# Performance work log

Hardware: AMD Instinct MI355X
Metric: run time of the kernel (lower is better)

Reference implementation:

```python
import jax, jax.numpy as jnp
import numpy as np

PAST = 15        # sum(num_classes[:-1])
NC = 20          # sum(num_classes)
ALPHA = 0.99
IGNORE = 255


def setup_inputs() -> dict:
    key = jax.random.key(0)
    k1, k2, k3, k4, k5, k6 = jax.random.split(key, 6)
    B, C, H, W = 8, NC, 512, 512
    logit = jax.random.normal(k1, (B, C, H, W), dtype=jnp.float32)
    # ema_prob is used as probabilities (gathered & compared to thresholds)
    ema_prob = jax.nn.softmax(jax.random.normal(k2, (B, C, H, W), dtype=jnp.float32), axis=1)
    ema_thresh = jax.random.uniform(k3, (NC,), dtype=jnp.float32, minval=0.2, maxval=0.8)
    real_labels = jax.random.randint(k4, (B, H, W), 0, NC, dtype=jnp.int64)
    # sprinkle ignore pixels (255) like real segmentation masks
    real_labels = jnp.where(jax.random.uniform(k5, (B, H, W)) < 0.1, IGNORE, real_labels)
    moving_prob_avg = jax.random.uniform(k6, (NC,), dtype=jnp.float32)
    return {"logit": logit, "ema_prob": ema_prob, "ema_thresh": ema_thresh,
            "real_labels": real_labels, "moving_prob_avg": moving_prob_avg}


def reference(logit, ema_prob, ema_thresh, real_labels, moving_prob_avg):
    # --- pseudo-labels from current model (detached softmax) ---
    logit_prob = jax.nn.softmax(jax.lax.stop_gradient(logit), axis=1)  # [B,C,H,W]
    labels = jnp.argmax(logit_prob[:, :PAST], axis=1)                   # [B,H,W]
    labels = jnp.where(real_labels >= PAST, real_labels, labels)
    idx = jnp.where(real_labels == IGNORE, 0, labels)
    scores = jnp.take_along_axis(logit_prob, idx[:, None], axis=1)[:, 0]  # [B,H,W]

    # --- per-class mean of scores + EMA update of moving_prob_avg ---
    flat_lab = labels.reshape(-1)
    flat_sc = scores.reshape(-1)
    seg = jnp.where(flat_lab == IGNORE, NC, flat_lab)  # route ignored to extra bucket
    sums = jax.ops.segment_sum(flat_sc, seg, num_segments=NC + 1)[:NC]
    counts = jax.ops.segment_sum(jnp.ones_like(flat_sc), seg, num_segments=NC + 1)[:NC]
    means = sums / jnp.maximum(counts, 1.0)
    mpa = moving_prob_avg  # numpy buffer in torch (no grad)
    new_mpa = jnp.where(counts > 0,
                        jnp.where(mpa == -1.0, means, (1.0 - ALPHA) * means + ALPHA * mpa),
                        mpa)

    # --- EMA-teacher pseudo labels + threshold mask ---
    ema_labels = jnp.argmax(ema_prob[:, :PAST], axis=1)
    ema_labels = jnp.where(real_labels >= PAST, real_labels, ema_labels)
    eidx = jnp.where(real_labels == IGNORE, 0, ema_labels)
    ema_scores = jnp.take_along_axis(ema_prob, eidx[:, None], axis=1)[:, 0]
    valid_cls = ema_labels < NC  # 255 never matches any class in the torch loop
    thr = ema_thresh[jnp.clip(ema_labels, 0, NC - 1)]
    ema_mask = valid_cls & (ema_scores >= thr)
    dynamic_labels = jnp.where(ema_mask, ema_labels, IGNORE)  # [B,H,W]

    # --- masked cross-entropy with per-class reweighting ---
    logp = jax.nn.log_softmax(logit, axis=1)
    cidx = jnp.clip(dynamic_labels, 0, NC - 1)
    losses = -jnp.take_along_axis(logp, cidx[:, None], axis=1)[:, 0]
    valid = dynamic_labels != IGNORE
    mult = jnp.where(valid, 1.0 - new_mpa[cidx], 1.0)
    losses = losses * jax.lax.stop_gradient(mult)  # multiplier is a host scalar in torch
    vs = valid.astype(losses.dtype)
    return jnp.sum(losses * vs) / jnp.sum(vs)
```

## Files before the change

kernel.cpp:

```cpp
#include <hip/hip_runtime.h>
#include <math.h>


#define PASTC 15
#define NCC   20
#define IGN   255
#define HW2   262144
#define ALPHAF 0.99f

#define TPX   256
#define NBLK  1024
#define ITER  8

typedef const __attribute__((address_space(1))) void* gp1_t;
typedef __attribute__((address_space(3))) void*       sp3_t;

__global__ __launch_bounds__(256) void dl_main(
    const float* __restrict__ logit,
    const float* __restrict__ ema,
    const float* __restrict__ thresh,
    const int*   __restrict__ real,
    float*       __restrict__ ws)
{
    __shared__ float stage[40 * TPX];
    __shared__ float s_acc[61];

    const int tid = threadIdx.x;
    const int wv  = tid >> 6;
    const int ln  = tid & 63;
    if (tid < 61) s_acc[tid] = 0.0f;

    for (int it = 0; it < ITER; ++it) {
        const int tile = blockIdx.x * ITER + it;
        const int p0   = tile * TPX;
        const int b    = p0 >> 18;
        const int s0   = p0 & (HW2 - 1);
        const size_t cb = ((size_t)(b * NCC) << 18) + (size_t)s0;

#pragma unroll
        for (int k = 0; k < 10; ++k) {
            const int e  = wv * 10 + k;
            const int tn = (e >= NCC);
            const int ch = tn ? (e - NCC) : e;
            const float* src = (tn ? ema : logit) + cb + ((size_t)ch << 18)
                             + (size_t)ln * 4;
            __builtin_amdgcn_global_load_lds((gp1_t)src, (sp3_t)&stage[e * TPX],
                                             16, 0, 0);
        }
        const int rl = real[p0 + tid];

        __syncthreads();

        const float* le = &stage[NCC * TPX];

        float e_m15 = le[tid]; int e_arg = 0;
#pragma unroll
        for (int c = 1; c < PASTC; ++c) {
            const float v = le[c * TPX + tid];
            if (v > e_m15) { e_m15 = v; e_arg = c; }
        }
        const int   el  = (rl >= PASTC) ? rl : e_arg;
        const float esc = (rl == IGN) ? le[tid]
                        : ((rl >= PASTC) ? le[rl * TPX + tid] : e_m15);
        const float th  = thresh[el < NCC ? el : (NCC - 1)];
        const bool  valid = (el < NCC) && (esc >= th);
        const int   cidx  = valid ? el : -1;

        float m20 = stage[tid], m15 = stage[tid]; int arg15 = 0;
#pragma unroll
        for (int c = 1; c < NCC; ++c) {
            const float v = stage[c * TPX + tid];
            if (c < PASTC && v > m15) { m15 = v; arg15 = c; }
            m20 = fmaxf(m20, v);
        }
        float se = 0.0f;
#pragma unroll
        for (int c = 0; c < NCC; ++c)
            se += __expf(stage[c * TPX + tid] - m20);
        const float lse = m20 + __logf(se);

        if (rl != IGN) {
            const int   lab  = (rl >= PASTC) ? rl : arg15;
            const float sval = (rl >= PASTC) ? stage[rl * TPX + tid] : m15;
            const float prob = __expf(sval - lse);
            atomicAdd(&s_acc[lab], prob);
            atomicAdd(&s_acc[20 + lab], 1.0f);
        }
        if (cidx >= 0) {
            const float capL = stage[cidx * TPX + tid];
            atomicAdd(&s_acc[40 + cidx], lse - capL);
        }
        const unsigned long long bm = __ballot(cidx >= 0);
        if (ln == 0) atomicAdd(&s_acc[60], (float)__popcll(bm));

        __syncthreads();
    }

    if (tid < 61) atomicAdd(&ws[tid], s_acc[tid]);
}

__global__ void dl_final(const float* __restrict__ ws,
                         const float* __restrict__ mpa,
                         float*       __restrict__ out)
{
    if (threadIdx.x == 0 && blockIdx.x == 0) {
        float acc = 0.0f;
        for (int c = 0; c < NCC; ++c) {
            const float ssum = ws[c];
            const float cnt  = ws[20 + c];
            const float lsum = ws[40 + c];
            const float m    = mpa[c];
            const float mean = ssum / fmaxf(cnt, 1.0f);
            const float nm   = (cnt > 0.0f)
                                 ? ((m == -1.0f) ? mean
                                                 : (1.0f - ALPHAF) * mean + ALPHAF * m)
                                 : m;
            acc += lsum * (1.0f - nm);
        }
        out[0] = acc / ws[60];
    }
}

extern "C" void kernel_launch(void* const* d_in, const int* in_sizes, int n_in,
                              void* d_out, int out_size, void* d_ws, size_t ws_size,
                              hipStream_t stream) {
    const float* logit  = (const float*)d_in[0];
    const float* ema    = (const float*)d_in[1];
    const float* thresh = (const float*)d_in[2];
    const int*   real   = (const int*)d_in[3];
    const float* mpa    = (const float*)d_in[4];
    float* out = (float*)d_out;
    float* ws  = (float*)d_ws;

    hipMemsetAsync(ws, 0, 64 * sizeof(float), stream);

    dl_main<<<NBLK, 256, 0, stream>>>(logit, ema, thresh, real, ws);
    dl_final<<<1, 64, 0, stream>>>(ws, mpa, out);
}
```

Baseline: 367.5 us.

## Split staging into separate ema and logit buffers and software-pipeline their loads

New measurement: 376.9 us. 2.5% more time.

```diff
diff --git a/kernel.cpp b/kernel.cpp
--- a/kernel.cpp
+++ b/kernel.cpp
@@ -15,6 +15,9 @@
 typedef const __attribute__((address_space(1))) void* gp1_t;
 typedef __attribute__((address_space(3))) void*       sp3_t;
 
+#define BARSYNC() asm volatile("s_waitcnt lgkmcnt(0)\n\ts_barrier" ::: "memory")
+#define WAITV(n)  asm volatile("s_waitcnt vmcnt(" #n ")" ::: "memory")
+
 __global__ __launch_bounds__(256) void dl_main(
     const float* __restrict__ logit,
     const float* __restrict__ ema,
@@ -22,80 +25,110 @@
     const int*   __restrict__ real,
     float*       __restrict__ ws)
 {
-    __shared__ float stage[40 * TPX];
+    __shared__ float bufE[NCC * TPX];
+    __shared__ float bufL[NCC * TPX];
+    __shared__ int   realrow[TPX];
     __shared__ float s_acc[61];
+    __shared__ float s_th[NCC];
 
     const int tid = threadIdx.x;
     const int wv  = tid >> 6;
     const int ln  = tid & 63;
-    if (tid < 61) s_acc[tid] = 0.0f;
+    if (tid < 61)  s_acc[tid] = 0.0f;
+    if (tid < NCC) s_th[tid]  = thresh[tid];
 
-    for (int it = 0; it < ITER; ++it) {
-        const int tile = blockIdx.x * ITER + it;
-        const int p0   = tile * TPX;
-        const int b    = p0 >> 18;
-        const int s0   = p0 & (HW2 - 1);
+    auto issue_ema = [&](int tile) {
+        const int p0 = tile * TPX;
+        const int b  = p0 >> 18;
+        const int s0 = p0 & (HW2 - 1);
         const size_t cb = ((size_t)(b * NCC) << 18) + (size_t)s0;
+#pragma unroll
+        for (int k2 = 0; k2 < 5; ++k2) {
+            const int ch = wv * 5 + k2;
+            const float* src = ema + cb + ((size_t)ch << 18) + (size_t)ln * 4;
+            __builtin_amdgcn_global_load_lds((gp1_t)src, (sp3_t)&bufE[ch * TPX], 16, 0, 0);
+        }
+        const int* rsrc = real + p0 + wv * 64 + ln;
+        __builtin_amdgcn_global_load_lds((gp1_t)rsrc, (sp3_t)&realrow[wv * 64], 4, 0, 0);
+    };
+    auto issue_logit = [&](int tile) {
+        const int p0 = tile * TPX;
+        const int b  = p0 >> 18;
+        const int s0 = p0 & (HW2 - 1);
+        const size_t cb = ((size_t)(b * NCC) << 18) + (size_t)s0;
+#pragma unroll
+        for (int k2 = 0; k2 < 5; ++k2) {
+            const int ch = wv * 5 + k2;
+            const float* src = logit + cb + ((size_t)ch << 18) + (size_t)ln * 4;
+            __builtin_amdgcn_global_load_lds((gp1_t)src, (sp3_t)&bufL[ch * TPX], 16, 0, 0);
+        }
+    };
 
-#pragma unroll
-        for (int k = 0; k < 10; ++k) {
-            const int e  = wv * 10 + k;
-            const int tn = (e >= NCC);
-            const int ch = tn ? (e - NCC) : e;
-            const float* src = (tn ? ema : logit) + cb + ((size_t)ch << 18)
-                             + (size_t)ln * 4;
-            __builtin_amdgcn_global_load_lds((gp1_t)src, (sp3_t)&stage[e * TPX],
-                                             16, 0, 0);
-        }
-        const int rl = real[p0 + tid];
+    const int t0 = blockIdx.x * ITER;
+    issue_ema(t0);
 
-        __syncthreads();
+    int   rl = 0, cidx = -1;
 
-        const float* le = &stage[NCC * TPX];
+    for (int k = 0; k < ITER; ++k) {
+        issue_logit(t0 + k);
+        WAITV(5);
+        BARSYNC();
 
-        float e_m15 = le[tid]; int e_arg = 0;
+        rl = realrow[tid];
+        float e_m15 = bufE[tid]; int e_arg = 0;
 #pragma unroll
         for (int c = 1; c < PASTC; ++c) {
-            const float v = le[c * TPX + tid];
+            const float v = bufE[c * TPX + tid];
             if (v > e_m15) { e_m15 = v; e_arg = c; }
         }
-        const int   el  = (rl >= PASTC) ? rl : e_arg;
-        const float esc = (rl == IGN) ? le[tid]
-                        : ((rl >= PASTC) ? le[rl * TPX + tid] : e_m15);
-        const float th  = thresh[el < NCC ? el : (NCC - 1)];
-        const bool  valid = (el < NCC) && (esc >= th);
-        const int   cidx  = valid ? el : -1;
+        {
+            const int   el  = (rl >= PASTC) ? rl : e_arg;
+            const int   gch = (rl == IGN) ? 0 : ((rl >= PASTC) ? rl : 0);
+            const float gv  = bufE[gch * TPX + tid];
+            const float esc = (rl != IGN && rl < PASTC) ? e_m15 : gv;
+            const float th  = s_th[el < NCC ? el : (NCC - 1)];
+            cidx = ((el < NCC) && (esc >= th)) ? el : -1;
+        }
+        BARSYNC();
 
-        float m20 = stage[tid], m15 = stage[tid]; int arg15 = 0;
+        if (k < ITER - 1) { issue_ema(t0 + k + 1); WAITV(6); }
+        else              { WAITV(0); }
+        BARSYNC();
+
+        float m20 = bufL[tid], m15v = bufL[tid]; int arg15 = 0;
 #pragma unroll
         for (int c = 1; c < NCC; ++c) {
-            const float v = stage[c * TPX + tid];
-            if (c < PASTC && v > m15) { m15 = v; arg15 = c; }
+            const float v = bufL[c * TPX + tid];
+            if (c < PASTC && v > m15v) { m15v = v; arg15 = c; }
             m20 = fmaxf(m20, v);
         }
         float se = 0.0f;
 #pragma unroll
         for (int c = 0; c < NCC; ++c)
-            se += __expf(stage[c * TPX + tid] - m20);
+            se += __expf(bufL[c * TPX + tid] - m20);
         const float lse = m20 + __logf(se);
 
         if (rl != IGN) {
             const int   lab  = (rl >= PASTC) ? rl : arg15;
-            const float sval = (rl >= PASTC) ? stage[rl * TPX + tid] : m15;
+            const int   sch  = (rl >= PASTC && rl < NCC) ? rl : 0;
+            const float sg   = bufL[sch * TPX + tid];
+            const float sval = (rl >= PASTC) ? sg : m15v;
             const float prob = __expf(sval - lse);
             atomicAdd(&s_acc[lab], prob);
             atomicAdd(&s_acc[20 + lab], 1.0f);
         }
-        if (cidx >= 0) {
-            const float capL = stage[cidx * TPX + tid];
-            atomicAdd(&s_acc[40 + cidx], lse - capL);
+        {
+            const int   cch  = (cidx >= 0) ? cidx : 0;
+            const float capL = bufL[cch * TPX + tid];
+            if (cidx >= 0) atomicAdd(&s_acc[40 + cidx], lse - capL);
         }
         const unsigned long long bm = __ballot(cidx >= 0);
         if (ln == 0) atomicAdd(&s_acc[60], (float)__popcll(bm));
 
-        __syncthreads();
+        BARSYNC();
     }
 
+    __syncthreads();
     if (tid < 61) atomicAdd(&ws[tid], s_acc[tid]);
 }
 
```
